# Performance work log

Hardware: AMD Instinct MI355X
Metric: run time of the kernel (lower is better)

Reference implementation:

```python
import jax, jax.numpy as jnp
import numpy as np


def setup_inputs() -> dict:
    key = jax.random.key(0)
    ks = jax.random.split(key, 9)
    B, Nq, Nkv, C, ICO = 1, 512, 2562, 64, 64
    return {
        "q": jax.random.normal(ks[0], (B, Nq, C), jnp.float32),
        "q_coord": jax.random.normal(ks[1], (B, Nq, 3), jnp.float32),
        "kv": jax.random.normal(ks[2], (B, Nkv, ICO), jnp.float32),
        "kv_coord": jax.random.normal(ks[3], (B, Nkv, 3), jnp.float32),
        "Wq": jax.random.normal(ks[4], (C, C), jnp.float32) * (C ** -0.5),
        "Wkv": jax.random.normal(ks[5], (ICO, 2 * C), jnp.float32) * (ICO ** -0.5),
        "Wdelta": jax.random.normal(ks[6], (3, C), jnp.float32) * (3 ** -0.5),
        "Wproj": jax.random.normal(ks[7], (C, C), jnp.float32) * (C ** -0.5),
        "bproj": jnp.zeros((C,), jnp.float32),
    }


def reference(q, q_coord, kv, kv_coord, Wq, Wkv, Wdelta, Wproj, bproj):
    C = q.shape[-1]
    scale = 1.0 / C  # erp_dim ** -1 (qk_scale=None)
    q_ = q @ Wq                                   # [B, Nq, C]
    kv_ = kv @ Wkv                                # [B, Nkv, 2C]
    k, v = jnp.split(kv_, 2, axis=-1)             # each [B, Nkv, C]
    # positional encoding: exp(-|dq - dk|) over 3D coords, projected to C
    pos_enc = jnp.exp(-jnp.abs(q_coord[:, :, None] - kv_coord[:, None])) @ Wdelta  # [B,Nq,Nkv,C]
    # elementwise abs-diff attention score, reduced over channel dim
    score = (jnp.exp(-jnp.abs(q_[:, :, None] - k[:, None])) + pos_enc).sum(-1) * scale  # [B,Nq,Nkv]
    attn = jax.nn.softmax(score, axis=-1)
    out = attn @ v                                # [B, Nq, C]
    return out @ Wproj + bproj
```

## Files before the change

### kernel.cpp

```cpp
#include <hip/hip_runtime.h>

#define NQ   512
#define NKV  2562
#define CH   64
#define QB   2
#define BT   512
#define NJQ  4
#define JQ   641
#define PSTRIDE 132
#define LOG2E 1.44269504088896340736f

#define KVROWS 8
#define NKVB ((NKV + KVROWS - 1) / KVROWS)
#define QROWS 16
#define NQB (NQ / QROWS)

#define E2(a, b) exp2f(-fabsf((a) - (b)))

__global__ __launch_bounds__(256) void gemm_qkv(
    const float* __restrict__ q, const float* __restrict__ kv,
    const float* __restrict__ Wq, const float* __restrict__ Wkv,
    float* __restrict__ qp, float* __restrict__ kvp) {
  const int tid = threadIdx.x;
  if (blockIdx.x < NKVB) {
    const int j0 = blockIdx.x * KVROWS;
    __shared__ float s_in[KVROWS][CH];
    if (tid < KVROWS * (CH / 4)) {
      int r = tid >> 4, g = tid & 15;
      int j = j0 + r;
      float4 v = (j < NKV) ? ((const float4*)(kv + (size_t)j * CH))[g]
                           : make_float4(0.f, 0.f, 0.f, 0.f);
      ((float4*)&s_in[r][0])[g] = v;
    }
    __syncthreads();
    const int r = tid >> 5;
    const int mg = (tid & 31) * 4;
    float4 acc = make_float4(0.f, 0.f, 0.f, 0.f);
#pragma unroll 16
    for (int rr = 0; rr < CH; ++rr) {
      float a = s_in[r][rr];
      float4 w = *(const float4*)(Wkv + (size_t)rr * 2 * CH + mg);
      acc.x = fmaf(a, w.x, acc.x); acc.y = fmaf(a, w.y, acc.y);
      acc.z = fmaf(a, w.z, acc.z); acc.w = fmaf(a, w.w, acc.w);
    }
    if (mg < CH) {
      acc.x *= LOG2E; acc.y *= LOG2E; acc.z *= LOG2E; acc.w *= LOG2E;
    }
    int j = j0 + r;
    if (j < NKV) *(float4*)(kvp + (size_t)j * 2 * CH + mg) = acc;
  } else {
    const int i0 = (blockIdx.x - NKVB) * QROWS;
    __shared__ float s_in[QROWS][CH];
    {
      int r = tid >> 4, g = tid & 15;
      float4 v = ((const float4*)(q + (size_t)(i0 + r) * CH))[g];
      ((float4*)&s_in[r][0])[g] = v;
    }
    __syncthreads();
    const int r = tid >> 4;
    const int cg = (tid & 15) * 4;
    float4 acc = make_float4(0.f, 0.f, 0.f, 0.f);
#pragma unroll 16
    for (int rr = 0; rr < CH; ++rr) {
      float a = s_in[r][rr];
      float4 w = *(const float4*)(Wq + (size_t)rr * CH + cg);
      acc.x = fmaf(a, w.x, acc.x); acc.y = fmaf(a, w.y, acc.y);
      acc.z = fmaf(a, w.z, acc.z); acc.w = fmaf(a, w.w, acc.w);
    }
    acc.x *= LOG2E; acc.y *= LOG2E; acc.z *= LOG2E; acc.w *= LOG2E;
    *(float4*)(qp + (size_t)(i0 + r) * CH + cg) = acc;
  }
}

__global__ __launch_bounds__(BT, 4) void attn_part(
    const float* __restrict__ qp, const float* __restrict__ kvp,
    const float* __restrict__ qc, const float* __restrict__ kvc,
    const float* __restrict__ Wdelta, float* __restrict__ part) {
  __shared__ float s_score[QB][JQ];
  __shared__ float s_red[QB][BT];
  __shared__ float s_wd[3];

  const int qpair = blockIdx.x >> 2;
  const int h = blockIdx.x & 3;
  const int i0 = qpair * QB;
  const int jlo = h * JQ;
  const int jhi = (jlo + JQ < NKV) ? jlo + JQ : NKV;

  const int tid = threadIdx.x;
  const int sub = tid & 3;
  const int c0 = sub * 16;
  const int wid = tid >> 6;
  const int lane = tid & 63;

  if (tid < 3) {
    float s = 0.f;
    for (int c = 0; c < CH; ++c) s += Wdelta[tid * CH + c];
    s_wd[tid] = s;
  }

  const float4* q0p = (const float4*)(qp + (size_t)i0 * CH + c0);
  const float4* q1p = (const float4*)(qp + (size_t)(i0 + 1) * CH + c0);
  float4 qa0 = q0p[0], qa1 = q0p[1], qa2 = q0p[2], qa3 = q0p[3];
  float4 qb0 = q1p[0], qb1 = q1p[1], qb2 = q1p[2], qb3 = q1p[3];
  asm volatile("" : "+v"(qa0.x), "+v"(qa0.y), "+v"(qa0.z), "+v"(qa0.w),
                    "+v"(qa1.x), "+v"(qa1.y), "+v"(qa1.z), "+v"(qa1.w),
                    "+v"(qa2.x), "+v"(qa2.y), "+v"(qa2.z), "+v"(qa2.w),
                    "+v"(qa3.x), "+v"(qa3.y), "+v"(qa3.z), "+v"(qa3.w));
  asm volatile("" : "+v"(qb0.x), "+v"(qb0.y), "+v"(qb0.z), "+v"(qb0.w),
                    "+v"(qb1.x), "+v"(qb1.y), "+v"(qb1.z), "+v"(qb1.w),
                    "+v"(qb2.x), "+v"(qb2.y), "+v"(qb2.z), "+v"(qb2.w),
                    "+v"(qb3.x), "+v"(qb3.y), "+v"(qb3.z), "+v"(qb3.w));

  float qc0[3], qc1[3];
#pragma unroll
  for (int d = 0; d < 3; ++d) {
    qc0[d] = qc[(size_t)i0 * 3 + d] * LOG2E;
    qc1[d] = qc[(size_t)(i0 + 1) * 3 + d] * LOG2E;
  }
  __syncthreads();
  const float wd0 = s_wd[0], wd1 = s_wd[1], wd2 = s_wd[2];
  const float pscale = (1.0f / 64.0f) * LOG2E;

  float ls0 = 0.f, ls1 = 0.f;
  for (int j = jlo + (tid >> 2); j < jhi; j += BT / 4) {
    const float4* kr = (const float4*)(kvp + (size_t)j * 2 * CH + c0);
    float4 k0 = kr[0], k1 = kr[1], k2 = kr[2], k3 = kr[3];
    float s0 = ((E2(qa0.x, k0.x) + E2(qa0.y, k0.y)) + (E2(qa0.z, k0.z) + E2(qa0.w, k0.w)))
             + ((E2(qa1.x, k1.x) + E2(qa1.y, k1.y)) + (E2(qa1.z, k1.z) + E2(qa1.w, k1.w)))
             + ((E2(qa2.x, k2.x) + E2(qa2.y, k2.y)) + (E2(qa2.z, k2.z) + E2(qa2.w, k2.w)))
             + ((E2(qa3.x, k3.x) + E2(qa3.y, k3.y)) + (E2(qa3.z, k3.z) + E2(qa3.w, k3.w)));
    float s1 = ((E2(qb0.x, k0.x) + E2(qb0.y, k0.y)) + (E2(qb0.z, k0.z) + E2(qb0.w, k0.w)))
             + ((E2(qb1.x, k1.x) + E2(qb1.y, k1.y)) + (E2(qb1.z, k1.z) + E2(qb1.w, k1.w)))
             + ((E2(qb2.x, k2.x) + E2(qb2.y, k2.y)) + (E2(qb2.z, k2.z) + E2(qb2.w, k2.w)))
             + ((E2(qb3.x, k3.x) + E2(qb3.y, k3.y)) + (E2(qb3.z, k3.z) + E2(qb3.w, k3.w)));
    s0 += __shfl_xor(s0, 1); s0 += __shfl_xor(s0, 2);
    s1 += __shfl_xor(s1, 1); s1 += __shfl_xor(s1, 2);
    if (sub == 0) {
      float d0 = kvc[(size_t)j * 3 + 0] * LOG2E;
      float d1 = kvc[(size_t)j * 3 + 1] * LOG2E;
      float d2 = kvc[(size_t)j * 3 + 2] * LOG2E;
      s0 += E2(qc0[0], d0) * wd0 + E2(qc0[1], d1) * wd1 + E2(qc0[2], d2) * wd2;
      s1 += E2(qc1[0], d0) * wd0 + E2(qc1[1], d1) * wd1 + E2(qc1[2], d2) * wd2;
      float p0 = exp2f(s0 * pscale);
      float p1 = exp2f(s1 * pscale);
      s_score[0][j - jlo] = p0; s_score[1][j - jlo] = p1;
      ls0 += p0; ls1 += p1;
    }
  }

#pragma unroll
  for (int off = 1; off < 64; off <<= 1) {
    ls0 += __shfl_xor(ls0, off);
    ls1 += __shfl_xor(ls1, off);
  }
  if (lane == 0) { s_red[0][wid] = ls0; s_red[1][wid] = ls1; }
  __syncthreads();
  float t0 = s_red[0][0], t1 = s_red[1][0];
#pragma unroll
  for (int w = 1; w < BT / 64; ++w) { t0 += s_red[0][w]; t1 += s_red[1][w]; }
  __syncthreads();

  const int c = tid & 63, g = tid >> 6;
  float a0 = 0.f, a1 = 0.f;
#pragma unroll 4
  for (int j = jlo + g; j < jhi; j += 8) {
    float v = kvp[(size_t)j * 128 + 64 + c];
    a0 = fmaf(s_score[0][j - jlo], v, a0);
    a1 = fmaf(s_score[1][j - jlo], v, a1);
  }
  s_red[0][tid] = a0; s_red[1][tid] = a1;
  __syncthreads();

  float* P = part + (size_t)(qpair * NJQ + h) * PSTRIDE;
  if (g == 0) {
    float u0 = 0.f, u1 = 0.f;
#pragma unroll
    for (int gg = 0; gg < 8; ++gg) {
      u0 += s_red[0][gg * 64 + c];
      u1 += s_red[1][gg * 64 + c];
    }
    P[4 + c] = u0;
    P[68 + c] = u1;
    if (c == 0) { P[0] = t0; P[1] = t1; }
  }
}

__global__ __launch_bounds__(256) void attn_merge(
    const float* __restrict__ part, const float* __restrict__ Wproj,
    const float* __restrict__ bproj, float* __restrict__ out) {
  __shared__ float s_o[4][CH];
  const int tid = threadIdx.x;
  const int g = tid >> 6, c = tid & 63;
  const int i = blockIdx.x * 4 + g;
  const int qpi = i >> 1, qs = i & 1;

  float ssum = 0.f, osum = 0.f;
#pragma unroll
  for (int h = 0; h < NJQ; ++h) {
    const float* P = part + (size_t)(qpi * NJQ + h) * PSTRIDE;
    ssum += P[qs];
    osum += P[4 + qs * 64 + c];
  }
  s_o[g][c] = osum / ssum;
  __syncthreads();

  float acc = 0.f;
#pragma unroll 16
  for (int r = 0; r < CH; ++r)
    acc = fmaf(s_o[g][r], Wproj[r * CH + c], acc);
  out[(size_t)i * CH + c] = acc + bproj[c];
}

extern "C" void kernel_launch(void* const* d_in, const int* in_sizes, int n_in,
                              void* d_out, int out_size, void* d_ws, size_t ws_size,
                              hipStream_t stream) {
  const float* q      = (const float*)d_in[0];
  const float* qc     = (const float*)d_in[1];
  const float* kv     = (const float*)d_in[2];
  const float* kvc    = (const float*)d_in[3];
  const float* Wq     = (const float*)d_in[4];
  const float* Wkv    = (const float*)d_in[5];
  const float* Wdelta = (const float*)d_in[6];
  const float* Wproj  = (const float*)d_in[7];
  const float* bproj  = (const float*)d_in[8];
  float* outp = (float*)d_out;

  float* qp   = (float*)d_ws;
  float* kvp  = qp + NQ * CH;
  float* part = kvp + (size_t)NKV * 2 * CH;

  gemm_qkv<<<NKVB + NQB, 256, 0, stream>>>(q, kv, Wq, Wkv, qp, kvp);
  attn_part<<<(NQ / QB) * NJQ, BT, 0, stream>>>(qp, kvp, qc, kvc, Wdelta, part);
  attn_merge<<<NQ / 4, 256, 0, stream>>>(part, Wproj, bproj, outp);
}
```

Before: 119.9 us.

## Prefetch next K row, pre-pack scaled kv coords, use raw v_exp_f32

The score loop now software-pipelines its global loads, fetching the next K row and coordinate float4 while computing the current one. kv coordinates are pre-scaled by log2e and padded to float4 in the projection kernel, so each lane reads them with one vector load. exp2f is replaced by inline v_exp_f32 with the -abs modifier folded in, and the P·V loop unroll goes from 4 to 8. The prefetch raises register pressure, and the raw exp skips exp2f's denormal range handling.

After: 106.5 us. 1.13x faster.

```diff
diff --git a/kernel.cpp b/kernel.cpp
--- a/kernel.cpp
+++ b/kernel.cpp
@@ -14,13 +14,21 @@
 #define NKVB ((NKV + KVROWS - 1) / KVROWS)
 #define QROWS 16
 #define NQB (NQ / QROWS)
-
-#define E2(a, b) exp2f(-fabsf((a) - (b)))
+#define NCB  41
+
+static __device__ __forceinline__ float exp2_raw(float x) {
+  float r; asm("v_exp_f32 %0, %1" : "=v"(r) : "v"(x)); return r;
+}
+static __device__ __forceinline__ float exp2_negabs(float x) {
+  float r; asm("v_exp_f32 %0, -abs(%1)" : "=v"(r) : "v"(x)); return r;
+}
+#define E2(a, b) exp2_negabs((a) - (b))
 
 __global__ __launch_bounds__(256) void gemm_qkv(
     const float* __restrict__ q, const float* __restrict__ kv,
     const float* __restrict__ Wq, const float* __restrict__ Wkv,
-    float* __restrict__ qp, float* __restrict__ kvp) {
+    const float* __restrict__ kvc, float* __restrict__ qp,
+    float* __restrict__ kvp, float* __restrict__ kvc4) {
   const int tid = threadIdx.x;
   if (blockIdx.x < NKVB) {
     const int j0 = blockIdx.x * KVROWS;
@@ -48,7 +56,7 @@
     }
     int j = j0 + r;
     if (j < NKV) *(float4*)(kvp + (size_t)j * 2 * CH + mg) = acc;
-  } else {
+  } else if (blockIdx.x < NKVB + NQB) {
     const int i0 = (blockIdx.x - NKVB) * QROWS;
     __shared__ float s_in[QROWS][CH];
     {
@@ -69,12 +77,18 @@
     }
     acc.x *= LOG2E; acc.y *= LOG2E; acc.z *= LOG2E; acc.w *= LOG2E;
     *(float4*)(qp + (size_t)(i0 + r) * CH + cg) = acc;
+  } else {
+    int t = (blockIdx.x - NKVB - NQB) * 256 + tid;
+    if (t < NKV * 4) {
+      int j = t >> 2, d = t & 3;
+      kvc4[t] = (d < 3) ? kvc[(size_t)j * 3 + d] * LOG2E : 0.f;
+    }
   }
 }
 
 __global__ __launch_bounds__(BT, 4) void attn_part(
     const float* __restrict__ qp, const float* __restrict__ kvp,
-    const float* __restrict__ qc, const float* __restrict__ kvc,
+    const float* __restrict__ qc, const float* __restrict__ kvc4,
     const float* __restrict__ Wdelta, float* __restrict__ part) {
   __shared__ float s_score[QB][JQ];
   __shared__ float s_red[QB][BT];
@@ -121,10 +135,23 @@
   const float wd0 = s_wd[0], wd1 = s_wd[1], wd2 = s_wd[2];
   const float pscale = (1.0f / 64.0f) * LOG2E;
 
+  const int step = BT / 4;
   float ls0 = 0.f, ls1 = 0.f;
-  for (int j = jlo + (tid >> 2); j < jhi; j += BT / 4) {
-    const float4* kr = (const float4*)(kvp + (size_t)j * 2 * CH + c0);
-    float4 k0 = kr[0], k1 = kr[1], k2 = kr[2], k3 = kr[3];
+  int j = jlo + (tid >> 2);
+  float4 k0, k1, k2, k3, cc;
+  {
+    int jc = (j < jhi) ? j : jlo;
+    const float4* kr = (const float4*)(kvp + (size_t)jc * 128 + c0);
+    k0 = kr[0]; k1 = kr[1]; k2 = kr[2]; k3 = kr[3];
+    cc = *(const float4*)(kvc4 + (size_t)jc * 4);
+  }
+  while (j < jhi) {
+    const int jn = j + step;
+    const int jnc = (jn < jhi) ? jn : jlo;
+    const float4* krn = (const float4*)(kvp + (size_t)jnc * 128 + c0);
+    float4 n0 = krn[0], n1 = krn[1], n2 = krn[2], n3 = krn[3];
+    float4 cn = *(const float4*)(kvc4 + (size_t)jnc * 4);
+
     float s0 = ((E2(qa0.x, k0.x) + E2(qa0.y, k0.y)) + (E2(qa0.z, k0.z) + E2(qa0.w, k0.w)))
              + ((E2(qa1.x, k1.x) + E2(qa1.y, k1.y)) + (E2(qa1.z, k1.z) + E2(qa1.w, k1.w)))
              + ((E2(qa2.x, k2.x) + E2(qa2.y, k2.y)) + (E2(qa2.z, k2.z) + E2(qa2.w, k2.w)))
@@ -136,16 +163,15 @@
     s0 += __shfl_xor(s0, 1); s0 += __shfl_xor(s0, 2);
     s1 += __shfl_xor(s1, 1); s1 += __shfl_xor(s1, 2);
     if (sub == 0) {
-      float d0 = kvc[(size_t)j * 3 + 0] * LOG2E;
-      float d1 = kvc[(size_t)j * 3 + 1] * LOG2E;
-      float d2 = kvc[(size_t)j * 3 + 2] * LOG2E;
-      s0 += E2(qc0[0], d0) * wd0 + E2(qc0[1], d1) * wd1 + E2(qc0[2], d2) * wd2;
-      s1 += E2(qc1[0], d0) * wd0 + E2(qc1[1], d1) * wd1 + E2(qc1[2], d2) * wd2;
-      float p0 = exp2f(s0 * pscale);
-      float p1 = exp2f(s1 * pscale);
+      s0 += E2(qc0[0], cc.x) * wd0 + E2(qc0[1], cc.y) * wd1 + E2(qc0[2], cc.z) * wd2;
+      s1 += E2(qc1[0], cc.x) * wd0 + E2(qc1[1], cc.y) * wd1 + E2(qc1[2], cc.z) * wd2;
+      float p0 = exp2_raw(s0 * pscale);
+      float p1 = exp2_raw(s1 * pscale);
       s_score[0][j - jlo] = p0; s_score[1][j - jlo] = p1;
       ls0 += p0; ls1 += p1;
     }
+    k0 = n0; k1 = n1; k2 = n2; k3 = n3; cc = cn;
+    j = jn;
   }
 
 #pragma unroll
@@ -162,11 +188,11 @@
 
   const int c = tid & 63, g = tid >> 6;
   float a0 = 0.f, a1 = 0.f;
-#pragma unroll 4
-  for (int j = jlo + g; j < jhi; j += 8) {
-    float v = kvp[(size_t)j * 128 + 64 + c];
-    a0 = fmaf(s_score[0][j - jlo], v, a0);
-    a1 = fmaf(s_score[1][j - jlo], v, a1);
+#pragma unroll 8
+  for (int j2 = jlo + g; j2 < jhi; j2 += 8) {
+    float v = kvp[(size_t)j2 * 128 + 64 + c];
+    a0 = fmaf(s_score[0][j2 - jlo], v, a0);
+    a1 = fmaf(s_score[1][j2 - jlo], v, a1);
   }
   s_red[0][tid] = a0; s_red[1][tid] = a1;
   __syncthreads();
@@ -228,8 +254,9 @@
   float* qp   = (float*)d_ws;
   float* kvp  = qp + NQ * CH;
   float* part = kvp + (size_t)NKV * 2 * CH;
-
-  gemm_qkv<<<NKVB + NQB, 256, 0, stream>>>(q, kv, Wq, Wkv, qp, kvp);
-  attn_part<<<(NQ / QB) * NJQ, BT, 0, stream>>>(qp, kvp, qc, kvc, Wdelta, part);
+  float* kvc4 = part + (size_t)(NQ / QB) * NJQ * PSTRIDE;
+
+  gemm_qkv<<<NKVB + NQB + NCB, 256, 0, stream>>>(q, kv, Wq, Wkv, kvc, qp, kvp, kvc4);
+  attn_part<<<(NQ / QB) * NJQ, BT, 0, stream>>>(qp, kvp, qc, kvc4, Wdelta, part);
   attn_merge<<<NQ / 4, 256, 0, stream>>>(part, Wproj, bproj, outp);
 }
```

## Replace per-pair exp(-|q-k|) with min of precomputed exp products

Applied to the files above, without the earlier changes.

Uses the identity exp(-|a-b|) = min(e^a·e^-b, e^-a·e^b). The exponentials of q, k and the coordinates are computed once in the projection kernel and stored, with kv rows widened to hold e^k, e^-k and v. The inner score loop then does two multiplies and a min instead of a transcendental per element, removing the exp bottleneck. The attention kernel also drops to 256 threads with 8 lanes per key row, and it stores the transformed coordinates in a padded buffer. The risk is overflow or underflow of exp for large projected values, which would lose precision relative to the reference.

After: 110.4 us. 7.9% less time.

```diff
diff --git a/kernel.cpp b/kernel.cpp
--- a/kernel.cpp
+++ b/kernel.cpp
@@ -4,23 +4,29 @@
 #define NKV  2562
 #define CH   64
 #define QB   2
-#define BT   512
+#define BT   256
 #define NJQ  4
 #define JQ   641
 #define PSTRIDE 132
 #define LOG2E 1.44269504088896340736f
+#define KROW 192
 
 #define KVROWS 8
 #define NKVB ((NKV + KVROWS - 1) / KVROWS)
 #define QROWS 16
 #define NQB (NQ / QROWS)
-
-#define E2(a, b) exp2f(-fabsf((a) - (b)))
+#define NCB  81
+
+static __device__ __forceinline__ float exp2_raw(float x) {
+  float r; asm("v_exp_f32 %0, %1" : "=v"(r) : "v"(x)); return r;
+}
+#define TMIN(EQ, EQi, EK, EKi) fminf((EQ) * (EKi), (EQi) * (EK))
 
 __global__ __launch_bounds__(256) void gemm_qkv(
     const float* __restrict__ q, const float* __restrict__ kv,
     const float* __restrict__ Wq, const float* __restrict__ Wkv,
-    float* __restrict__ qp, float* __restrict__ kvp) {
+    const float* __restrict__ kvc, float* __restrict__ qp,
+    float* __restrict__ kvp, float* __restrict__ kvc8) {
   const int tid = threadIdx.x;
   if (blockIdx.x < NKVB) {
     const int j0 = blockIdx.x * KVROWS;
@@ -43,12 +49,21 @@
       acc.x = fmaf(a, w.x, acc.x); acc.y = fmaf(a, w.y, acc.y);
       acc.z = fmaf(a, w.z, acc.z); acc.w = fmaf(a, w.w, acc.w);
     }
-    if (mg < CH) {
-      acc.x *= LOG2E; acc.y *= LOG2E; acc.z *= LOG2E; acc.w *= LOG2E;
-    }
     int j = j0 + r;
-    if (j < NKV) *(float4*)(kvp + (size_t)j * 2 * CH + mg) = acc;
-  } else {
+    if (j < NKV) {
+      if (mg < CH) {
+        float4 ek, eki;
+        ek.x = exp2_raw(acc.x * LOG2E);  eki.x = exp2_raw(-acc.x * LOG2E);
+        ek.y = exp2_raw(acc.y * LOG2E);  eki.y = exp2_raw(-acc.y * LOG2E);
+        ek.z = exp2_raw(acc.z * LOG2E);  eki.z = exp2_raw(-acc.z * LOG2E);
+        ek.w = exp2_raw(acc.w * LOG2E);  eki.w = exp2_raw(-acc.w * LOG2E);
+        *(float4*)(kvp + (size_t)j * KROW + mg) = ek;
+        *(float4*)(kvp + (size_t)j * KROW + 64 + mg) = eki;
+      } else {
+        *(float4*)(kvp + (size_t)j * KROW + 64 + mg) = acc;
+      }
+    }
+  } else if (blockIdx.x < NKVB + NQB) {
     const int i0 = (blockIdx.x - NKVB) * QROWS;
     __shared__ float s_in[QROWS][CH];
     {
@@ -67,14 +82,28 @@
       acc.x = fmaf(a, w.x, acc.x); acc.y = fmaf(a, w.y, acc.y);
       acc.z = fmaf(a, w.z, acc.z); acc.w = fmaf(a, w.w, acc.w);
     }
-    acc.x *= LOG2E; acc.y *= LOG2E; acc.z *= LOG2E; acc.w *= LOG2E;
-    *(float4*)(qp + (size_t)(i0 + r) * CH + cg) = acc;
+    float4 eq, eqi;
+    eq.x = exp2_raw(acc.x * LOG2E);  eqi.x = exp2_raw(-acc.x * LOG2E);
+    eq.y = exp2_raw(acc.y * LOG2E);  eqi.y = exp2_raw(-acc.y * LOG2E);
+    eq.z = exp2_raw(acc.z * LOG2E);  eqi.z = exp2_raw(-acc.z * LOG2E);
+    eq.w = exp2_raw(acc.w * LOG2E);  eqi.w = exp2_raw(-acc.w * LOG2E);
+    *(float4*)(qp + (size_t)(i0 + r) * 128 + cg) = eq;
+    *(float4*)(qp + (size_t)(i0 + r) * 128 + 64 + cg) = eqi;
+  } else {
+    int t = (blockIdx.x - NKVB - NQB) * 256 + tid;
+    if (t < NKV * 8) {
+      int j = t >> 3, d = t & 7;
+      float val = 0.f;
+      if (d < 3)               val = exp2_raw( kvc[(size_t)j * 3 + d]      * LOG2E);
+      else if (d >= 4 && d < 7) val = exp2_raw(-kvc[(size_t)j * 3 + (d-4)] * LOG2E);
+      kvc8[t] = val;
+    }
   }
 }
 
 __global__ __launch_bounds__(BT, 4) void attn_part(
     const float* __restrict__ qp, const float* __restrict__ kvp,
-    const float* __restrict__ qc, const float* __restrict__ kvc,
+    const float* __restrict__ qc, const float* __restrict__ kvc8,
     const float* __restrict__ Wdelta, float* __restrict__ part) {
   __shared__ float s_score[QB][JQ];
   __shared__ float s_red[QB][BT];
@@ -87,8 +116,8 @@
   const int jhi = (jlo + JQ < NKV) ? jlo + JQ : NKV;
 
   const int tid = threadIdx.x;
-  const int sub = tid & 3;
-  const int c0 = sub * 16;
+  const int sub = tid & 7;
+  const int c0 = sub * 8;
   const int wid = tid >> 6;
   const int lane = tid & 63;
 
@@ -98,61 +127,76 @@
     s_wd[tid] = s;
   }
 
-  const float4* q0p = (const float4*)(qp + (size_t)i0 * CH + c0);
-  const float4* q1p = (const float4*)(qp + (size_t)(i0 + 1) * CH + c0);
-  float4 qa0 = q0p[0], qa1 = q0p[1], qa2 = q0p[2], qa3 = q0p[3];
-  float4 qb0 = q1p[0], qb1 = q1p[1], qb2 = q1p[2], qb3 = q1p[3];
+  const float4* pa  = (const float4*)(qp + (size_t)(i0 + 0) * 128 + c0);
+  const float4* pai = (const float4*)(qp + (size_t)(i0 + 0) * 128 + 64 + c0);
+  const float4* pb  = (const float4*)(qp + (size_t)(i0 + 1) * 128 + c0);
+  const float4* pbi = (const float4*)(qp + (size_t)(i0 + 1) * 128 + 64 + c0);
+  float4 qa0 = pa[0],  qa1 = pa[1];
+  float4 qA0 = pai[0], qA1 = pai[1];
+  float4 qb0 = pb[0],  qb1 = pb[1];
+  float4 qB0 = pbi[0], qB1 = pbi[1];
   asm volatile("" : "+v"(qa0.x), "+v"(qa0.y), "+v"(qa0.z), "+v"(qa0.w),
                     "+v"(qa1.x), "+v"(qa1.y), "+v"(qa1.z), "+v"(qa1.w),
-                    "+v"(qa2.x), "+v"(qa2.y), "+v"(qa2.z), "+v"(qa2.w),
-                    "+v"(qa3.x), "+v"(qa3.y), "+v"(qa3.z), "+v"(qa3.w));
+                    "+v"(qA0.x), "+v"(qA0.y), "+v"(qA0.z), "+v"(qA0.w),
+                    "+v"(qA1.x), "+v"(qA1.y), "+v"(qA1.z), "+v"(qA1.w));
   asm volatile("" : "+v"(qb0.x), "+v"(qb0.y), "+v"(qb0.z), "+v"(qb0.w),
                     "+v"(qb1.x), "+v"(qb1.y), "+v"(qb1.z), "+v"(qb1.w),
-                    "+v"(qb2.x), "+v"(qb2.y), "+v"(qb2.z), "+v"(qb2.w),
-                    "+v"(qb3.x), "+v"(qb3.y), "+v"(qb3.z), "+v"(qb3.w));
-
-  float qc0[3], qc1[3];
+                    "+v"(qB0.x), "+v"(qB0.y), "+v"(qB0.z), "+v"(qB0.w),
+                    "+v"(qB1.x), "+v"(qB1.y), "+v"(qB1.z), "+v"(qB1.w));
+
+  float ca[3], cA[3], cb[3], cB[3];
 #pragma unroll
   for (int d = 0; d < 3; ++d) {
-    qc0[d] = qc[(size_t)i0 * 3 + d] * LOG2E;
-    qc1[d] = qc[(size_t)(i0 + 1) * 3 + d] * LOG2E;
+    float v0 = qc[(size_t)(i0 + 0) * 3 + d] * LOG2E;
+    float v1 = qc[(size_t)(i0 + 1) * 3 + d] * LOG2E;
+    ca[d] = exp2_raw(v0);  cA[d] = exp2_raw(-v0);
+    cb[d] = exp2_raw(v1);  cB[d] = exp2_raw(-v1);
   }
   __syncthreads();
   const float wd0 = s_wd[0], wd1 = s_wd[1], wd2 = s_wd[2];
   const float pscale = (1.0f / 64.0f) * LOG2E;
 
   float ls0 = 0.f, ls1 = 0.f;
-  for (int j = jlo + (tid >> 2); j < jhi; j += BT / 4) {
-    const float4* kr = (const float4*)(kvp + (size_t)j * 2 * CH + c0);
-    float4 k0 = kr[0], k1 = kr[1], k2 = kr[2], k3 = kr[3];
-    float s0 = ((E2(qa0.x, k0.x) + E2(qa0.y, k0.y)) + (E2(qa0.z, k0.z) + E2(qa0.w, k0.w)))
-             + ((E2(qa1.x, k1.x) + E2(qa1.y, k1.y)) + (E2(qa1.z, k1.z) + E2(qa1.w, k1.w)))
-             + ((E2(qa2.x, k2.x) + E2(qa2.y, k2.y)) + (E2(qa2.z, k2.z) + E2(qa2.w, k2.w)))
-             + ((E2(qa3.x, k3.x) + E2(qa3.y, k3.y)) + (E2(qa3.z, k3.z) + E2(qa3.w, k3.w)));
-    float s1 = ((E2(qb0.x, k0.x) + E2(qb0.y, k0.y)) + (E2(qb0.z, k0.z) + E2(qb0.w, k0.w)))
-             + ((E2(qb1.x, k1.x) + E2(qb1.y, k1.y)) + (E2(qb1.z, k1.z) + E2(qb1.w, k1.w)))
-             + ((E2(qb2.x, k2.x) + E2(qb2.y, k2.y)) + (E2(qb2.z, k2.z) + E2(qb2.w, k2.w)))
-             + ((E2(qb3.x, k3.x) + E2(qb3.y, k3.y)) + (E2(qb3.z, k3.z) + E2(qb3.w, k3.w)));
-    s0 += __shfl_xor(s0, 1); s0 += __shfl_xor(s0, 2);
-    s1 += __shfl_xor(s1, 1); s1 += __shfl_xor(s1, 2);
+  for (int j = jlo + (tid >> 3); j < jhi; j += BT / 8) {
+    const float4* ek  = (const float4*)(kvp + (size_t)j * KROW + c0);
+    const float4* eki = (const float4*)(kvp + (size_t)j * KROW + 64 + c0);
+    float4 k0 = ek[0], k1 = ek[1];
+    float4 K0 = eki[0], K1 = eki[1];
+
+    float s0 = ((TMIN(qa0.x, qA0.x, k0.x, K0.x) + TMIN(qa0.y, qA0.y, k0.y, K0.y))
+             +  (TMIN(qa0.z, qA0.z, k0.z, K0.z) + TMIN(qa0.w, qA0.w, k0.w, K0.w)))
+             + ((TMIN(qa1.x, qA1.x, k1.x, K1.x) + TMIN(qa1.y, qA1.y, k1.y, K1.y))
+             +  (TMIN(qa1.z, qA1.z, k1.z, K1.z) + TMIN(qa1.w, qA1.w, k1.w, K1.w)));
+    float s1 = ((TMIN(qb0.x, qB0.x, k0.x, K0.x) + TMIN(qb0.y, qB0.y, k0.y, K0.y))
+             +  (TMIN(qb0.z, qB0.z, k0.z, K0.z) + TMIN(qb0.w, qB0.w, k0.w, K0.w)))
+             + ((TMIN(qb1.x, qB1.x, k1.x, K1.x) + TMIN(qb1.y, qB1.y, k1.y, K1.y))
+             +  (TMIN(qb1.z, qB1.z, k1.z, K1.z) + TMIN(qb1.w, qB1.w, k1.w, K1.w)));
+    s0 += __shfl_xor(s0, 1); s0 += __shfl_xor(s0, 2); s0 += __shfl_xor(s0, 4);
+    s1 += __shfl_xor(s1, 1); s1 += __shfl_xor(s1, 2); s1 += __shfl_xor(s1, 4);
     if (sub == 0) {
-      float d0 = kvc[(size_t)j * 3 + 0] * LOG2E;
-      float d1 = kvc[(size_t)j * 3 + 1] * LOG2E;
-      float d2 = kvc[(size_t)j * 3 + 2] * LOG2E;
-      s0 += E2(qc0[0], d0) * wd0 + E2(qc0[1], d1) * wd1 + E2(qc0[2], d2) * wd2;
-      s1 += E2(qc1[0], d0) * wd0 + E2(qc1[1], d1) * wd1 + E2(qc1[2], d2) * wd2;
-      float p0 = exp2f(s0 * pscale);
-      float p1 = exp2f(s1 * pscale);
-      s_score[0][j - jlo] = p0; s_score[1][j - jlo] = p1;
+      float4 kc  = *(const float4*)(kvc8 + (size_t)j * 8);
+      float4 kci = *(const float4*)(kvc8 + (size_t)j * 8 + 4);
+      s0 += TMIN(ca[0], cA[0], kc.x, kci.x) * wd0
+          + TMIN(ca[1], cA[1], kc.y, kci.y) * wd1
+          + TMIN(ca[2], cA[2], kc.z, kci.z) * wd2;
+      s1 += TMIN(cb[0], cB[0], kc.x, kci.x) * wd0
+          + TMIN(cb[1], cB[1], kc.y, kci.y) * wd1
+          + TMIN(cb[2], cB[2], kc.z, kci.z) * wd2;
+      float p0 = exp2_raw(s0 * pscale);
+      float p1 = exp2_raw(s1 * pscale);
+      int jj = j - jlo;
+      s_score[0][jj] = p0; s_score[1][jj] = p1;
       ls0 += p0; ls1 += p1;
     }
   }
 
 #pragma unroll
-  for (int off = 1; off < 64; off <<= 1) {
+  for (int off = 8; off < 64; off <<= 1) {
     ls0 += __shfl_xor(ls0, off);
     ls1 += __shfl_xor(ls1, off);
   }
+  ls0 += __shfl_xor(ls0, 1); ls0 += __shfl_xor(ls0, 2); ls0 += __shfl_xor(ls0, 4);
+  ls1 += __shfl_xor(ls1, 1); ls1 += __shfl_xor(ls1, 2); ls1 += __shfl_xor(ls1, 4);
   if (lane == 0) { s_red[0][wid] = ls0; s_red[1][wid] = ls1; }
   __syncthreads();
   float t0 = s_red[0][0], t1 = s_red[1][0];
@@ -162,11 +206,12 @@
 
   const int c = tid & 63, g = tid >> 6;
   float a0 = 0.f, a1 = 0.f;
-#pragma unroll 4
-  for (int j = jlo + g; j < jhi; j += 8) {
-    float v = kvp[(size_t)j * 128 + 64 + c];
-    a0 = fmaf(s_score[0][j - jlo], v, a0);
-    a1 = fmaf(s_score[1][j - jlo], v, a1);
+#pragma unroll 8
+  for (int j2 = jlo + g; j2 < jhi; j2 += 4) {
+    float v = kvp[(size_t)j2 * KROW + 128 + c];
+    int jj = j2 - jlo;
+    a0 = fmaf(s_score[0][jj], v, a0);
+    a1 = fmaf(s_score[1][jj], v, a1);
   }
   s_red[0][tid] = a0; s_red[1][tid] = a1;
   __syncthreads();
@@ -175,7 +220,7 @@
   if (g == 0) {
     float u0 = 0.f, u1 = 0.f;
 #pragma unroll
-    for (int gg = 0; gg < 8; ++gg) {
+    for (int gg = 0; gg < 4; ++gg) {
       u0 += s_red[0][gg * 64 + c];
       u1 += s_red[1][gg * 64 + c];
     }
@@ -226,10 +271,11 @@
   float* outp = (float*)d_out;
 
   float* qp   = (float*)d_ws;
-  float* kvp  = qp + NQ * CH;
-  float* part = kvp + (size_t)NKV * 2 * CH;
-
-  gemm_qkv<<<NKVB + NQB, 256, 0, stream>>>(q, kv, Wq, Wkv, qp, kvp);
-  attn_part<<<(NQ / QB) * NJQ, BT, 0, stream>>>(qp, kvp, qc, kvc, Wdelta, part);
+  float* kvp  = qp + (size_t)NQ * 128;
+  float* part = kvp + (size_t)NKV * KROW;
+  float* kvc8 = part + (size_t)(NQ / QB) * NJQ * PSTRIDE;
+
+  gemm_qkv<<<NKVB + NQB + NCB, 256, 0, stream>>>(q, kv, Wq, Wkv, kvc, qp, kvp, kvc8);
+  attn_part<<<(NQ / QB) * NJQ, BT, 0, stream>>>(qp, kvp, qc, kvc8, Wdelta, part);
   attn_merge<<<NQ / 4, 256, 0, stream>>>(part, Wproj, bproj, outp);
 }
```
